# Kernel tuning notes

Hardware: AMD Instinct MI355X
Metric: run time of the kernel (lower is better)

Reference implementation:

```python
import jax, jax.numpy as jnp
import numpy as np

B, T, IN, H = 512, 512, 1, 64


def _lstm_dir(x, w_ih, w_hh, b_ih, b_hh, reverse):
    """Single-direction LSTM over x:[B,T,D]. PyTorch gate order i,f,g,o."""
    # Precompute input contribution for all timesteps (one big GEMM).
    xg = jnp.einsum('btd,gd->btg', x, w_ih) + (b_ih + b_hh)  # [B,T,4H]
    if reverse:
        xg = xg[:, ::-1]
    Hh = w_hh.shape[1]
    w_hh_t = w_hh.T  # [H,4H]

    def step(carry, g_t):
        h, c = carry
        g = g_t + h @ w_hh_t  # [B,4H]
        i, f, gc, o = jnp.split(g, 4, axis=-1)
        c = jax.nn.sigmoid(f) * c + jax.nn.sigmoid(i) * jnp.tanh(gc)
        h = jax.nn.sigmoid(o) * jnp.tanh(c)
        return (h, c), h

    b = x.shape[0]
    init = (jnp.zeros((b, Hh), x.dtype), jnp.zeros((b, Hh), x.dtype))
    _, hs = jax.lax.scan(step, init, jnp.swapaxes(xg, 0, 1))  # hs:[T,B,H]
    hs = jnp.swapaxes(hs, 0, 1)  # [B,T,H]
    return hs[:, ::-1] if reverse else hs


def _bilstm_layer(x, wf, rf, bf, bf2, wr, rr, br, br2):
    fwd = _lstm_dir(x, wf, rf, bf, bf2, reverse=False)
    bwd = _lstm_dir(x, wr, rr, br, br2, reverse=True)
    return jnp.concatenate([fwd, bwd], axis=-1)  # [B,T,2H]


def setup_inputs() -> dict:
    key = jax.random.key(0)
    ks = jax.random.split(key, 20)
    s = 1.0 / np.sqrt(H)
    u = lambda k, shape: jax.random.uniform(k, shape, jnp.float32, -s, s)
    inp = {'x': jax.random.normal(ks[0], (B, T, IN), jnp.float32)}
    # layer 0 (input dim IN), layer 1 (input dim 2H), fwd and reverse dirs
    inp['w_ih_l0'] = u(ks[1], (4 * H, IN)); inp['w_hh_l0'] = u(ks[2], (4 * H, H))
    inp['b_ih_l0'] = u(ks[3], (4 * H,));   inp['b_hh_l0'] = u(ks[4], (4 * H,))
    inp['w_ih_l0r'] = u(ks[5], (4 * H, IN)); inp['w_hh_l0r'] = u(ks[6], (4 * H, H))
    inp['b_ih_l0r'] = u(ks[7], (4 * H,));    inp['b_hh_l0r'] = u(ks[8], (4 * H,))
    inp['w_ih_l1'] = u(ks[9], (4 * H, 2 * H)); inp['w_hh_l1'] = u(ks[10], (4 * H, H))
    inp['b_ih_l1'] = u(ks[11], (4 * H,));      inp['b_hh_l1'] = u(ks[12], (4 * H,))
    inp['w_ih_l1r'] = u(ks[13], (4 * H, 2 * H)); inp['w_hh_l1r'] = u(ks[14], (4 * H, H))
    inp['b_ih_l1r'] = u(ks[15], (4 * H,));       inp['b_hh_l1r'] = u(ks[16], (4 * H,))
    inp['fc_w'] = u(ks[17], (1, 2 * H)); inp['fc_b'] = u(ks[18], (1,))
    return inp


def reference(x, w_ih_l0, w_hh_l0, b_ih_l0, b_hh_l0,
              w_ih_l0r, w_hh_l0r, b_ih_l0r, b_hh_l0r,
              w_ih_l1, w_hh_l1, b_ih_l1, b_hh_l1,
              w_ih_l1r, w_hh_l1r, b_ih_l1r, b_hh_l1r,
              fc_w, fc_b):
    h0 = _bilstm_layer(x, w_ih_l0, w_hh_l0, b_ih_l0, b_hh_l0,
                       w_ih_l0r, w_hh_l0r, b_ih_l0r, b_hh_l0r)
    h1 = _bilstm_layer(h0, w_ih_l1, w_hh_l1, b_ih_l1, b_hh_l1,
                       w_ih_l1r, w_hh_l1r, b_ih_l1r, b_hh_l1r)
    last = h1[:, -1, :]  # [B,2H]
    return last @ fc_w.T + fc_b  # [B,1]
```

## Files before the change

kernel.cpp:

```cpp
#include <hip/hip_runtime.h>
#include <cstddef>
#include <cstdint>

#define Tn 512
#define Bn 512

__device__ __forceinline__ float rlane(float v, int lane) {
    return __uint_as_float((unsigned)__builtin_amdgcn_readlane((int)__float_as_uint(v), lane));
}
__device__ __forceinline__ float sigm(float x) { return 1.0f / (1.0f + __expf(-x)); }
__device__ __forceinline__ float tanhf_(float x) { return 1.0f - 2.0f / (1.0f + __expf(2.0f * x)); }

#define BAR_LGKM() asm volatile("s_waitcnt lgkmcnt(0)\n\ts_barrier" ::: "memory")

__global__ __launch_bounds__(64, 1) void k_lstm_l0(
    const float* __restrict__ x,
    const float* __restrict__ wih_f, const float* __restrict__ whh_f,
    const float* __restrict__ bih_f, const float* __restrict__ bhh_f,
    const float* __restrict__ wih_r, const float* __restrict__ whh_r,
    const float* __restrict__ bih_r, const float* __restrict__ bhh_r,
    float* __restrict__ h0out)
{
    const int j   = threadIdx.x;
    const int bp  = blockIdx.x >> 1;
    const int dir = blockIdx.x & 1;
    const int b0  = bp * 2;
    const int b1  = b0 + 1;

    const float* __restrict__ wih = dir ? wih_r : wih_f;
    const float* __restrict__ whh = dir ? whh_r : whh_f;
    const float* __restrict__ bih = dir ? bih_r : bih_f;
    const float* __restrict__ bhh = dir ? bhh_r : bhh_f;

    __shared__ float xs[2][Tn];
    #pragma unroll
    for (int i = 0; i < Tn / 64; ++i) {
        xs[0][i * 64 + j] = x[(size_t)b0 * Tn + i * 64 + j];
        xs[1][i * 64 + j] = x[(size_t)b1 * Tn + i * 64 + j];
    }

    float w[4][64];
    float wx[4], bias[4];
    #pragma unroll
    for (int g = 0; g < 4; ++g) {
        const int r = g * 64 + j;
        wx[g]   = wih[r];
        bias[g] = bih[r] + bhh[r];
        #pragma unroll
        for (int k4 = 0; k4 < 16; ++k4) {
            const float4 v = *reinterpret_cast<const float4*>(&whh[(size_t)r * 64 + k4 * 4]);
            w[g][k4 * 4 + 0] = v.x; w[g][k4 * 4 + 1] = v.y;
            w[g][k4 * 4 + 2] = v.z; w[g][k4 * 4 + 3] = v.w;
        }
    }

    float hA = 0.0f, cA = 0.0f, hB = 0.0f, cB = 0.0f;
    float* __restrict__ opA = h0out + (size_t)b0 * Tn * 128 + dir * 64 + j;
    float* __restrict__ opB = h0out + (size_t)b1 * Tn * 128 + dir * 64 + j;

    for (int s = 0; s < Tn; ++s) {
        const int t = dir ? (Tn - 1 - s) : s;
        const float xtA = xs[0][t];
        const float xtB = xs[1][t];

        float aA0 = fmaf(xtA, wx[0], bias[0]);
        float aA1 = fmaf(xtA, wx[1], bias[1]);
        float aA2 = fmaf(xtA, wx[2], bias[2]);
        float aA3 = fmaf(xtA, wx[3], bias[3]);
        float aB0 = fmaf(xtB, wx[0], bias[0]);
        float aB1 = fmaf(xtB, wx[1], bias[1]);
        float aB2 = fmaf(xtB, wx[2], bias[2]);
        float aB3 = fmaf(xtB, wx[3], bias[3]);
        #pragma unroll
        for (int k = 0; k < 64; ++k) {
            const float vA = rlane(hA, k);
            const float vB = rlane(hB, k);
            const float w0 = w[0][k], w1 = w[1][k], w2 = w[2][k], w3 = w[3][k];
            aA0 = fmaf(vA, w0, aA0);  aB0 = fmaf(vB, w0, aB0);
            aA1 = fmaf(vA, w1, aA1);  aB1 = fmaf(vB, w1, aB1);
            aA2 = fmaf(vA, w2, aA2);  aB2 = fmaf(vB, w2, aB2);
            aA3 = fmaf(vA, w3, aA3);  aB3 = fmaf(vB, w3, aB3);
        }
        cA = sigm(aA1) * cA + sigm(aA0) * tanhf_(aA2);
        hA = sigm(aA3) * tanhf_(cA);
        cB = sigm(aB1) * cB + sigm(aB0) * tanhf_(aB2);
        hB = sigm(aB3) * tanhf_(cB);
        opA[(size_t)t * 128] = hA;
        opB[(size_t)t * 128] = hB;
    }
}

__global__ __launch_bounds__(512, 2) void k_lstm_l1f(
    const float* __restrict__ h0,
    const float* __restrict__ wih, const float* __restrict__ whh,
    const float* __restrict__ bih, const float* __restrict__ bhh,
    float* __restrict__ h1last)
{
    const int tid = threadIdx.x;
    const int e   = tid >> 8;
    const int wv  = (tid >> 6) & 3;
    const int j   = tid & 63;
    const int b   = blockIdx.x * 2 + e;
    const int kbase = wv * 48;

    __shared__ float4 part[2][2][4][64];

    float bias[4];
    #pragma unroll
    for (int g = 0; g < 4; ++g) {
        const int r = g * 64 + j;
        bias[g] = bih[r] + bhh[r];
    }

    float wt[4][48];
    #pragma unroll
    for (int g = 0; g < 4; ++g) {
        const int r = g * 64 + j;
        #pragma unroll
        for (int k4 = 0; k4 < 12; ++k4) {
            const int k = kbase + k4 * 4;
            const float* __restrict__ src = (k < 128)
                ? (wih + (size_t)r * 128 + k)
                : (whh + (size_t)r * 64 + (k - 128));
            const float4 w4 = *reinterpret_cast<const float4*>(src);
            wt[g][k4 * 4 + 0] = w4.x; wt[g][k4 * 4 + 1] = w4.y;
            wt[g][k4 * 4 + 2] = w4.z; wt[g][k4 * 4 + 3] = w4.w;
        }
    }

    const float* __restrict__ xrow = h0 + (size_t)b * Tn * 128;

    float x1a = 0.0f, x1b = 0.0f;
    if (wv <= 1) x1a = xrow[j];
    if (wv == 1 || wv == 2) x1b = xrow[64 + j];
    float h = 0.0f, c = 0.0f;

    for (int t = 0; t < Tn; ++t) {
        const int bf = t & 1;
        const int tn = (t + 1 < Tn) ? (t + 1) : t;
        float nx1a = x1a, nx1b = x1b;
        if (wv <= 1)            nx1a = xrow[(size_t)tn * 128 + j];
        if (wv == 1 || wv == 2) nx1b = xrow[(size_t)tn * 128 + 64 + j];

        float a0 = 0.0f, a1 = 0.0f, a2 = 0.0f, a3 = 0.0f;
        if (wv == 0) {
            #pragma unroll
            for (int kk = 0; kk < 48; ++kk) {
                const float v = rlane(x1a, kk);
                a0 = fmaf(v, wt[0][kk], a0); a1 = fmaf(v, wt[1][kk], a1);
                a2 = fmaf(v, wt[2][kk], a2); a3 = fmaf(v, wt[3][kk], a3);
            }
        } else if (wv == 1) {
            #pragma unroll
            for (int kk = 0; kk < 48; ++kk) {
                const float v = (kk < 16) ? rlane(x1a, 48 + kk) : rlane(x1b, kk - 16);
                a0 = fmaf(v, wt[0][kk], a0); a1 = fmaf(v, wt[1][kk], a1);
                a2 = fmaf(v, wt[2][kk], a2); a3 = fmaf(v, wt[3][kk], a3);
            }
        } else if (wv == 2) {
            #pragma unroll
            for (int kk = 0; kk < 48; ++kk) {
                const float v = (kk < 32) ? rlane(x1b, 32 + kk) : rlane(h, kk - 32);
                a0 = fmaf(v, wt[0][kk], a0); a1 = fmaf(v, wt[1][kk], a1);
                a2 = fmaf(v, wt[2][kk], a2); a3 = fmaf(v, wt[3][kk], a3);
            }
        } else {
            #pragma unroll
            for (int kk = 0; kk < 48; ++kk) {
                const float v = rlane(h, 16 + kk);
                a0 = fmaf(v, wt[0][kk], a0); a1 = fmaf(v, wt[1][kk], a1);
                a2 = fmaf(v, wt[2][kk], a2); a3 = fmaf(v, wt[3][kk], a3);
            }
        }
        part[e][bf][wv][j] = make_float4(a0, a1, a2, a3);
        BAR_LGKM();
        if (wv >= 2) {
            const float4 q0 = part[e][bf][0][j];
            const float4 q1 = part[e][bf][1][j];
            const float4 q2 = part[e][bf][2][j];
            const float4 q3 = part[e][bf][3][j];
            const float gi = bias[0] + q0.x + q1.x + q2.x + q3.x;
            const float gf = bias[1] + q0.y + q1.y + q2.y + q3.y;
            const float gg = bias[2] + q0.z + q1.z + q2.z + q3.z;
            const float go = bias[3] + q0.w + q1.w + q2.w + q3.w;
            c = sigm(gf) * c + sigm(gi) * tanhf_(gg);
            h = sigm(go) * tanhf_(c);
        }
        x1a = nx1a; x1b = nx1b;
    }
    if (wv == 2) h1last[(size_t)b * 64 + j] = h;
}

__global__ __launch_bounds__(64, 1) void k_l1r_fc(
    const float* __restrict__ h0in,
    const float* __restrict__ wihr,
    const float* __restrict__ bihr, const float* __restrict__ bhhr,
    const float* __restrict__ h1last,
    const float* __restrict__ fcw, const float* __restrict__ fcb,
    float* __restrict__ out)
{
    const int b = blockIdx.x;
    const int j = threadIdx.x;
    const float* __restrict__ xrow = h0in + ((size_t)b * Tn + (Tn - 1)) * 128;
    const float x1a = xrow[j];
    const float x1b = xrow[64 + j];
    float acc[4];
    #pragma unroll
    for (int g = 0; g < 4; ++g) {
        const int r = g * 64 + j;
        float a = bihr[r] + bhhr[r];
        const float* __restrict__ wr = wihr + (size_t)r * 128;
        #pragma unroll
        for (int d4 = 0; d4 < 16; ++d4) {
            const float4 w4 = *reinterpret_cast<const float4*>(&wr[d4 * 4]);
            a = fmaf(rlane(x1a, d4 * 4 + 0), w4.x, a);
            a = fmaf(rlane(x1a, d4 * 4 + 1), w4.y, a);
            a = fmaf(rlane(x1a, d4 * 4 + 2), w4.z, a);
            a = fmaf(rlane(x1a, d4 * 4 + 3), w4.w, a);
        }
        #pragma unroll
        for (int d4 = 0; d4 < 16; ++d4) {
            const float4 w4 = *reinterpret_cast<const float4*>(&wr[64 + d4 * 4]);
            a = fmaf(rlane(x1b, d4 * 4 + 0), w4.x, a);
            a = fmaf(rlane(x1b, d4 * 4 + 1), w4.y, a);
            a = fmaf(rlane(x1b, d4 * 4 + 2), w4.z, a);
            a = fmaf(rlane(x1b, d4 * 4 + 3), w4.w, a);
        }
        acc[g] = a;
    }
    const float cr = sigm(acc[0]) * tanhf_(acc[2]);
    const float hr = sigm(acc[3]) * tanhf_(cr);
    float v = h1last[(size_t)b * 64 + j] * fcw[j] + hr * fcw[64 + j];
    #pragma unroll
    for (int off = 32; off > 0; off >>= 1) v += __shfl_xor(v, off, 64);
    if (j == 0) out[b] = v + fcb[0];
}

extern "C" void kernel_launch(void* const* d_in, const int* in_sizes, int n_in,
                              void* d_out, int out_size, void* d_ws, size_t ws_size,
                              hipStream_t stream)
{
    const float* x       = (const float*)d_in[0];
    const float* wih_l0  = (const float*)d_in[1];
    const float* whh_l0  = (const float*)d_in[2];
    const float* bih_l0  = (const float*)d_in[3];
    const float* bhh_l0  = (const float*)d_in[4];
    const float* wih_l0r = (const float*)d_in[5];
    const float* whh_l0r = (const float*)d_in[6];
    const float* bih_l0r = (const float*)d_in[7];
    const float* bhh_l0r = (const float*)d_in[8];
    const float* wih_l1  = (const float*)d_in[9];
    const float* whh_l1  = (const float*)d_in[10];
    const float* bih_l1  = (const float*)d_in[11];
    const float* bhh_l1  = (const float*)d_in[12];
    const float* wih_l1r = (const float*)d_in[13];
    const float* whh_l1r = (const float*)d_in[14];
    const float* bih_l1r = (const float*)d_in[15];
    const float* bhh_l1r = (const float*)d_in[16];
    const float* fcw     = (const float*)d_in[17];
    const float* fcb     = (const float*)d_in[18];
    (void)whh_l1r; (void)in_sizes; (void)n_in; (void)out_size; (void)ws_size;

    float* h0     = (float*)d_ws;
    float* h1last = h0 + (size_t)Bn * Tn * 128;

    k_lstm_l0<<<dim3(Bn), dim3(64), 0, stream>>>(
        x, wih_l0, whh_l0, bih_l0, bhh_l0,
        wih_l0r, whh_l0r, bih_l0r, bhh_l0r, h0);
    k_lstm_l1f<<<dim3(Bn / 2), dim3(512), 0, stream>>>(
        h0, wih_l1, whh_l1, bih_l1, bhh_l1, h1last);
    k_l1r_fc<<<dim3(Bn), dim3(64), 0, stream>>>(
        h0, wih_l1r, bih_l1r, bhh_l1r, h1last, fcw, fcb, (float*)d_out);
}
```

Before: 1.373 ms.

## Use LDS float4 broadcast for hidden state and one batch per layer-0 block

Layer-0 now runs one batch row per 64-thread block and launches twice as many blocks. The recurrent hidden state is broadcast through shared memory as float4 loads instead of 64 readlane instructions per step. Layer-1 forward does the same for its h-dependent part, with h written to a per-wave LDS buffer. The aim is to cut the serial readlane/SGPR broadcast cost and raise parallelism, at the price of more blocks and LDS traffic. Layer-0 relies on single-wave lockstep, with no barrier between the h_lds write and the next read.

```diff
diff --git a/kernel.cpp b/kernel.cpp
--- a/kernel.cpp
+++ b/kernel.cpp
@@ -22,22 +22,19 @@
     float* __restrict__ h0out)
 {
     const int j   = threadIdx.x;
-    const int bp  = blockIdx.x >> 1;
+    const int b   = blockIdx.x >> 1;
     const int dir = blockIdx.x & 1;
-    const int b0  = bp * 2;
-    const int b1  = b0 + 1;
 
     const float* __restrict__ wih = dir ? wih_r : wih_f;
     const float* __restrict__ whh = dir ? whh_r : whh_f;
     const float* __restrict__ bih = dir ? bih_r : bih_f;
     const float* __restrict__ bhh = dir ? bhh_r : bhh_f;
 
-    __shared__ float xs[2][Tn];
-    #pragma unroll
-    for (int i = 0; i < Tn / 64; ++i) {
-        xs[0][i * 64 + j] = x[(size_t)b0 * Tn + i * 64 + j];
-        xs[1][i * 64 + j] = x[(size_t)b1 * Tn + i * 64 + j];
-    }
+    __shared__ float xs[Tn];
+    __shared__ __align__(16) float h_lds[64];
+
+    #pragma unroll
+    for (int i = 0; i < Tn / 64; ++i) xs[i * 64 + j] = x[(size_t)b * Tn + i * 64 + j];
 
     float w[4][64];
     float wx[4], bias[4];
@@ -53,40 +50,43 @@
             w[g][k4 * 4 + 2] = v.z; w[g][k4 * 4 + 3] = v.w;
         }
     }
-
-    float hA = 0.0f, cA = 0.0f, hB = 0.0f, cB = 0.0f;
-    float* __restrict__ opA = h0out + (size_t)b0 * Tn * 128 + dir * 64 + j;
-    float* __restrict__ opB = h0out + (size_t)b1 * Tn * 128 + dir * 64 + j;
+    h_lds[j] = 0.0f;
+
+    float h = 0.0f, c = 0.0f;
+    float* __restrict__ outp = h0out + (size_t)b * Tn * 128 + dir * 64 + j;
 
     for (int s = 0; s < Tn; ++s) {
         const int t = dir ? (Tn - 1 - s) : s;
-        const float xtA = xs[0][t];
-        const float xtB = xs[1][t];
-
-        float aA0 = fmaf(xtA, wx[0], bias[0]);
-        float aA1 = fmaf(xtA, wx[1], bias[1]);
-        float aA2 = fmaf(xtA, wx[2], bias[2]);
-        float aA3 = fmaf(xtA, wx[3], bias[3]);
-        float aB0 = fmaf(xtB, wx[0], bias[0]);
-        float aB1 = fmaf(xtB, wx[1], bias[1]);
-        float aB2 = fmaf(xtB, wx[2], bias[2]);
-        float aB3 = fmaf(xtB, wx[3], bias[3]);
-        #pragma unroll
-        for (int k = 0; k < 64; ++k) {
-            const float vA = rlane(hA, k);
-            const float vB = rlane(hB, k);
-            const float w0 = w[0][k], w1 = w[1][k], w2 = w[2][k], w3 = w[3][k];
-            aA0 = fmaf(vA, w0, aA0);  aB0 = fmaf(vB, w0, aB0);
-            aA1 = fmaf(vA, w1, aA1);  aB1 = fmaf(vB, w1, aB1);
-            aA2 = fmaf(vA, w2, aA2);  aB2 = fmaf(vB, w2, aB2);
-            aA3 = fmaf(vA, w3, aA3);  aB3 = fmaf(vB, w3, aB3);
-        }
-        cA = sigm(aA1) * cA + sigm(aA0) * tanhf_(aA2);
-        hA = sigm(aA3) * tanhf_(cA);
-        cB = sigm(aB1) * cB + sigm(aB0) * tanhf_(aB2);
-        hB = sigm(aB3) * tanhf_(cB);
-        opA[(size_t)t * 128] = hA;
-        opB[(size_t)t * 128] = hB;
+        const float xt = xs[t];
+
+        float a0 = fmaf(xt, wx[0], bias[0]);
+        float a1 = fmaf(xt, wx[1], bias[1]);
+        float a2 = fmaf(xt, wx[2], bias[2]);
+        float a3 = fmaf(xt, wx[3], bias[3]);
+        #pragma unroll
+        for (int k4 = 0; k4 < 16; ++k4) {
+            const float4 hv = *reinterpret_cast<const float4*>(&h_lds[k4 * 4]);
+            a0 = fmaf(hv.x, w[0][k4 * 4 + 0], a0);
+            a1 = fmaf(hv.x, w[1][k4 * 4 + 0], a1);
+            a2 = fmaf(hv.x, w[2][k4 * 4 + 0], a2);
+            a3 = fmaf(hv.x, w[3][k4 * 4 + 0], a3);
+            a0 = fmaf(hv.y, w[0][k4 * 4 + 1], a0);
+            a1 = fmaf(hv.y, w[1][k4 * 4 + 1], a1);
+            a2 = fmaf(hv.y, w[2][k4 * 4 + 1], a2);
+            a3 = fmaf(hv.y, w[3][k4 * 4 + 1], a3);
+            a0 = fmaf(hv.z, w[0][k4 * 4 + 2], a0);
+            a1 = fmaf(hv.z, w[1][k4 * 4 + 2], a1);
+            a2 = fmaf(hv.z, w[2][k4 * 4 + 2], a2);
+            a3 = fmaf(hv.z, w[3][k4 * 4 + 2], a3);
+            a0 = fmaf(hv.w, w[0][k4 * 4 + 3], a0);
+            a1 = fmaf(hv.w, w[1][k4 * 4 + 3], a1);
+            a2 = fmaf(hv.w, w[2][k4 * 4 + 3], a2);
+            a3 = fmaf(hv.w, w[3][k4 * 4 + 3], a3);
+        }
+        c = sigm(a1) * c + sigm(a0) * tanhf_(a2);
+        h = sigm(a3) * tanhf_(c);
+        h_lds[j] = h;
+        outp[(size_t)t * 128] = h;
     }
 }
 
@@ -104,6 +104,7 @@
     const int kbase = wv * 48;
 
     __shared__ float4 part[2][2][4][64];
+    __shared__ __align__(16) float hb[2][2][64];
 
     float bias[4];
     #pragma unroll
@@ -134,6 +135,8 @@
     if (wv <= 1) x1a = xrow[j];
     if (wv == 1 || wv == 2) x1b = xrow[64 + j];
     float h = 0.0f, c = 0.0f;
+    if (wv == 2) hb[e][0][j] = 0.0f;
+    if (wv == 3) hb[e][1][j] = 0.0f;
 
     for (int t = 0; t < Tn; ++t) {
         const int bf = t & 1;
@@ -159,17 +162,37 @@
             }
         } else if (wv == 2) {
             #pragma unroll
-            for (int kk = 0; kk < 48; ++kk) {
-                const float v = (kk < 32) ? rlane(x1b, 32 + kk) : rlane(h, kk - 32);
+            for (int kk = 0; kk < 32; ++kk) {
+                const float v = rlane(x1b, 32 + kk);
                 a0 = fmaf(v, wt[0][kk], a0); a1 = fmaf(v, wt[1][kk], a1);
                 a2 = fmaf(v, wt[2][kk], a2); a3 = fmaf(v, wt[3][kk], a3);
             }
+            #pragma unroll
+            for (int k4 = 0; k4 < 4; ++k4) {
+                const float4 hv = *reinterpret_cast<const float4*>(&hb[e][0][k4 * 4]);
+                const int kk = 32 + k4 * 4;
+                a0 = fmaf(hv.x, wt[0][kk + 0], a0); a1 = fmaf(hv.x, wt[1][kk + 0], a1);
+                a2 = fmaf(hv.x, wt[2][kk + 0], a2); a3 = fmaf(hv.x, wt[3][kk + 0], a3);
+                a0 = fmaf(hv.y, wt[0][kk + 1], a0); a1 = fmaf(hv.y, wt[1][kk + 1], a1);
+                a2 = fmaf(hv.y, wt[2][kk + 1], a2); a3 = fmaf(hv.y, wt[3][kk + 1], a3);
+                a0 = fmaf(hv.z, wt[0][kk + 2], a0); a1 = fmaf(hv.z, wt[1][kk + 2], a1);
+                a2 = fmaf(hv.z, wt[2][kk + 2], a2); a3 = fmaf(hv.z, wt[3][kk + 2], a3);
+                a0 = fmaf(hv.w, wt[0][kk + 3], a0); a1 = fmaf(hv.w, wt[1][kk + 3], a1);
+                a2 = fmaf(hv.w, wt[2][kk + 3], a2); a3 = fmaf(hv.w, wt[3][kk + 3], a3);
+            }
         } else {
             #pragma unroll
-            for (int kk = 0; kk < 48; ++kk) {
-                const float v = rlane(h, 16 + kk);
-                a0 = fmaf(v, wt[0][kk], a0); a1 = fmaf(v, wt[1][kk], a1);
-                a2 = fmaf(v, wt[2][kk], a2); a3 = fmaf(v, wt[3][kk], a3);
+            for (int k4 = 0; k4 < 12; ++k4) {
+                const float4 hv = *reinterpret_cast<const float4*>(&hb[e][1][16 + k4 * 4]);
+                const int kk = k4 * 4;
+                a0 = fmaf(hv.x, wt[0][kk + 0], a0); a1 = fmaf(hv.x, wt[1][kk + 0], a1);
+                a2 = fmaf(hv.x, wt[2][kk + 0], a2); a3 = fmaf(hv.x, wt[3][kk + 0], a3);
+                a0 = fmaf(hv.y, wt[0][kk + 1], a0); a1 = fmaf(hv.y, wt[1][kk + 1], a1);
+                a2 = fmaf(hv.y, wt[2][kk + 1], a2); a3 = fmaf(hv.y, wt[3][kk + 1], a3);
+                a0 = fmaf(hv.z, wt[0][kk + 2], a0); a1 = fmaf(hv.z, wt[1][kk + 2], a1);
+                a2 = fmaf(hv.z, wt[2][kk + 2], a2); a3 = fmaf(hv.z, wt[3][kk + 2], a3);
+                a0 = fmaf(hv.w, wt[0][kk + 3], a0); a1 = fmaf(hv.w, wt[1][kk + 3], a1);
+                a2 = fmaf(hv.w, wt[2][kk + 3], a2); a3 = fmaf(hv.w, wt[3][kk + 3], a3);
             }
         }
         part[e][bf][wv][j] = make_float4(a0, a1, a2, a3);
@@ -185,6 +208,7 @@
             const float go = bias[3] + q0.w + q1.w + q2.w + q3.w;
             c = sigm(gf) * c + sigm(gi) * tanhf_(gg);
             h = sigm(go) * tanhf_(c);
+            hb[e][wv - 2][j] = h;
         }
         x1a = nx1a; x1b = nx1b;
     }
@@ -264,7 +288,7 @@
     float* h0     = (float*)d_ws;
     float* h1last = h0 + (size_t)Bn * Tn * 128;
 
-    k_lstm_l0<<<dim3(Bn), dim3(64), 0, stream>>>(
+    k_lstm_l0<<<dim3(Bn * 2), dim3(64), 0, stream>>>(
         x, wih_l0, whh_l0, bih_l0, bhh_l0,
         wih_l0r, whh_l0r, bih_l0r, bhh_l0r, h0);
     k_lstm_l1f<<<dim3(Bn / 2), dim3(512), 0, stream>>>(
```

Measured after the change: 1.403 ms. 1.02x slower.
